# Kernel optimization log

Measured on AMD Instinct MI355X. Metric: run time of the kernel, lower is better.

## Reference

```python
import jax, jax.numpy as jnp
import numpy as np

SCALES = (5, 15, 40)


def _hamilton(a, b):
    # a, b: (..., 4) quaternions in [w, x, y, z]
    aw, ax, ay, az = a[..., 0], a[..., 1], a[..., 2], a[..., 3]
    bw, bx, by, bz = b[..., 0], b[..., 1], b[..., 2], b[..., 3]
    return jnp.stack([
        aw * bw - ax * bx - ay * by - az * bz,
        aw * bx + ax * bw + ay * bz - az * by,
        aw * by - ax * bz + ay * bw + az * bx,
        aw * bz + ax * by - ay * bx + az * bw,
    ], axis=-1)


def _bearing_quaternions(xyz):
    # xyz: (B, F, P, 3) -> bearing quaternions (B, F, P, 4)
    bbox_min = xyz.min(axis=2)
    bbox_max = xyz.max(axis=2)
    centroids = (bbox_min + bbox_max) * 0.5  # (B, F, 3)
    d = xyz - centroids[:, :, None, :]
    d = d / jnp.clip(jnp.linalg.norm(d, axis=-1, keepdims=True), 1e-12)
    dot = jnp.clip(d[..., 1], -1.0 + 1e-7, 1.0 - 1e-7)
    half = jnp.arccos(dot) * 0.5
    axis = jnp.stack([d[..., 2], jnp.zeros_like(d[..., 0]), -d[..., 0]], axis=-1)
    axis = axis / jnp.clip(jnp.linalg.norm(axis, axis=-1, keepdims=True), 1e-12)
    s = jnp.sin(half)
    return jnp.stack([jnp.cos(half), axis[..., 0] * s, axis[..., 1] * s, axis[..., 2] * s], axis=-1)


def _torch_lower_median(x):
    flat = jnp.sort(x.reshape(-1))
    return flat[(flat.shape[0] - 1) // 2]


def _bearing_qcc_multiscale(points_4d, num_frames):
    B, F, P, _ = points_4d.shape
    xyz = points_4d[..., :3]  # (B, F, P, 3)
    bq = _bearing_quaternions(xyz)  # (B, F, P, 4)

    # Per-transition relative quaternion q_fwd = q_tgt * conj(q_src), vectorized over T = F-1
    conj_sign = jnp.array([1.0, -1.0, -1.0, -1.0], dtype=points_4d.dtype)
    q_src = bq[:, :-1] * conj_sign  # conj, (B, T, P, 4)
    q_tgt = bq[:, 1:]
    q_fwd = _hamilton(q_tgt, q_src)
    q_fwd = q_fwd / jnp.clip(jnp.linalg.norm(q_fwd, axis=-1, keepdims=True), 1e-12)

    # KNN on source-frame xyz for all transitions at once (topk is sorted desc,
    # so smaller-k neighborhoods are prefixes of the max-k result)
    pts = xyz[:, :-1]  # (B, T, P, 3)
    sq = jnp.sum(pts * pts, axis=-1)  # (B, T, P)
    neg_dist = 2.0 * jnp.einsum('btpc,btqc->btpq', pts, pts) - sq[..., :, None] - sq[..., None, :]
    kmax = max(SCALES)
    _, idx = jax.lax.top_k(neg_dist, kmax)  # (B, T, P, kmax)

    # Gather neighbor quaternions: (B, T, P, kmax, 4)
    b_ix = jnp.arange(B)[:, None, None, None]
    t_ix = jnp.arange(F - 1)[None, :, None, None]
    nbr_q = q_fwd[b_ix, t_ix, idx]

    dots = jnp.abs(jnp.sum(q_fwd[..., None, :] * nbr_q, axis=-1))
    dots = jnp.clip(dots, 0.0, 1.0 - 1e-7)
    geo = 2.0 * jnp.arccos(dots)  # (B, T, P, kmax)

    rigidities = []
    for k in SCALES:
        mean_inc = geo[..., :k].mean(axis=-1).mean(axis=1)  # (B, P)
        scale = jnp.clip(_torch_lower_median(mean_inc), 1e-6)
        rig = jnp.where(mean_inc.max() > 0,
                        jnp.exp(-mean_inc / scale),
                        jnp.ones_like(mean_inc))  # (B, P)
        rig = jnp.broadcast_to(rig[:, None, :], (B, F, P)).reshape(B, 1, F * P)
        rigidities.append(rig)
    return jnp.concatenate(rigidities, axis=1)  # (B, len(SCALES), F*P)


def setup_inputs() -> dict:
    key = jax.random.key(0)
    B, F, P = 2, 8, 2048
    points_4d = jax.random.normal(key, (B, F, P, 4), dtype=jnp.float32)
    return {"points_4d": points_4d, "num_frames": F}


def reference(points_4d, num_frames):
    return _bearing_qcc_multiscale(points_4d, num_frames)
```

## Files before the change

kernel.cpp:

```cpp
#include <hip/hip_runtime.h>
#include <math.h>

typedef unsigned long long u64;
typedef unsigned int u32;

#define B_ 2
#define F_ 8
#define P_ 2048
#define T_ 7
#define ROWS (B_*T_*P_)
#define SENT_OU 0xFFFFFFFFu

#define CED(arr,a,b) do { double _x=arr[a], _y=arr[b]; arr[a]=fmin(_x,_y); arr[b]=fmax(_x,_y); } while(0)

__device__ __forceinline__ void sort8d(double* k) {
  CED(k,0,1); CED(k,2,3); CED(k,4,5); CED(k,6,7);
  CED(k,0,2); CED(k,1,3); CED(k,4,6); CED(k,5,7);
  CED(k,1,2); CED(k,5,6);
  CED(k,0,4); CED(k,1,5); CED(k,2,6); CED(k,3,7);
  CED(k,2,4); CED(k,3,5);
  CED(k,1,2); CED(k,3,4); CED(k,5,6);
}

__device__ __forceinline__ void low8(double* A, const double* Bv) {
#pragma unroll
  for (int i = 0; i < 8; ++i) A[i] = fmin(A[i], Bv[7-i]);
#pragma unroll
  for (int st = 4; st >= 1; st >>= 1) {
#pragma unroll
    for (int i = 0; i < 8; ++i) {
      if ((i & st) == 0) { CED(A, i, i + st); }
    }
  }
}

__device__ __forceinline__ u32 bfly16_min_u32(u32 x) {
  u32 t;
  t = (u32)__builtin_amdgcn_update_dpp((int)x,(int)x,0x0B1,0xF,0xF,false); x = t<x?t:x;
  t = (u32)__builtin_amdgcn_update_dpp((int)x,(int)x,0x04E,0xF,0xF,false); x = t<x?t:x;
  t = (u32)__builtin_amdgcn_update_dpp((int)x,(int)x,0x141,0xF,0xF,false); x = t<x?t:x;
  t = (u32)__builtin_amdgcn_update_dpp((int)x,(int)x,0x140,0xF,0xF,false); x = t<x?t:x;
  return x;
}
__device__ __forceinline__ float bfly16_sum_f32(float x) {
  float t;
  t = __uint_as_float((u32)__builtin_amdgcn_update_dpp((int)__float_as_uint(x),(int)__float_as_uint(x),0x0B1,0xF,0xF,false)); x += t;
  t = __uint_as_float((u32)__builtin_amdgcn_update_dpp((int)__float_as_uint(x),(int)__float_as_uint(x),0x04E,0xF,0xF,false)); x += t;
  t = __uint_as_float((u32)__builtin_amdgcn_update_dpp((int)__float_as_uint(x),(int)__float_as_uint(x),0x141,0xF,0xF,false)); x += t;
  t = __uint_as_float((u32)__builtin_amdgcn_update_dpp((int)__float_as_uint(x),(int)__float_as_uint(x),0x140,0xF,0xF,false)); x += t;
  return x;
}

__global__ __launch_bounds__(256) void kA1_bbox(const float4* __restrict__ pts,
                                                float* __restrict__ cent) {
  int bf = blockIdx.x;
  const float4* base = pts + (size_t)bf * P_;
  int tid = threadIdx.x;
  float mnx =  INFINITY, mny =  INFINITY, mnz =  INFINITY;
  float mxx = -INFINITY, mxy = -INFINITY, mxz = -INFINITY;
#pragma unroll
  for (int i = 0; i < 8; ++i) {
    float4 v = base[tid + i*256];
    mnx=fminf(mnx,v.x); mny=fminf(mny,v.y); mnz=fminf(mnz,v.z);
    mxx=fmaxf(mxx,v.x); mxy=fmaxf(mxy,v.y); mxz=fmaxf(mxz,v.z);
  }
#pragma unroll
  for (int off = 32; off >= 1; off >>= 1) {
    mnx=fminf(mnx,__shfl_xor(mnx,off)); mny=fminf(mny,__shfl_xor(mny,off)); mnz=fminf(mnz,__shfl_xor(mnz,off));
    mxx=fmaxf(mxx,__shfl_xor(mxx,off)); mxy=fmaxf(mxy,__shfl_xor(mxy,off)); mxz=fmaxf(mxz,__shfl_xor(mxz,off));
  }
  __shared__ float red[4][6];
  int wid = tid >> 6, lane = tid & 63;
  if (lane == 0) { red[wid][0]=mnx; red[wid][1]=mny; red[wid][2]=mnz;
                   red[wid][3]=mxx; red[wid][4]=mxy; red[wid][5]=mxz; }
  __syncthreads();
  if (tid == 0) {
    mnx=fminf(fminf(red[0][0],red[1][0]),fminf(red[2][0],red[3][0]));
    mny=fminf(fminf(red[0][1],red[1][1]),fminf(red[2][1],red[3][1]));
    mnz=fminf(fminf(red[0][2],red[1][2]),fminf(red[2][2],red[3][2]));
    mxx=fmaxf(fmaxf(red[0][3],red[1][3]),fmaxf(red[2][3],red[3][3]));
    mxy=fmaxf(fmaxf(red[0][4],red[1][4]),fmaxf(red[2][4],red[3][4]));
    mxz=fmaxf(fmaxf(red[0][5],red[1][5]),fmaxf(red[2][5],red[3][5]));
    cent[bf*3 + 0] = (mnx+mxx)*0.5f;
    cent[bf*3 + 1] = (mny+mxy)*0.5f;
    cent[bf*3 + 2] = (mnz+mxz)*0.5f;
  }
}

__device__ __forceinline__ float4 bearing(float4 v, float cx, float cy, float cz) {
  float dx=v.x-cx, dy=v.y-cy, dz=v.z-cz;
  float n = sqrtf(((dx*dx) + dy*dy) + dz*dz);
  n = fmaxf(n, 1e-12f);
  float dxn = dx/n, dyn = dy/n, dzn = dz/n;
  float dotc = fminf(fmaxf(dyn, -0.99999990f), 0.99999990f);
  float half = acosf(dotc) * 0.5f;
  float an = sqrtf(dzn*dzn + dxn*dxn);
  an = fmaxf(an, 1e-12f);
  float axx = dzn/an, axz = (-dxn)/an;
  float s = sinf(half), w = cosf(half);
  return make_float4(w, axx*s, 0.f, axz*s);
}

__global__ __launch_bounds__(256) void kAB_qfwd(const float4* __restrict__ pts,
                                                const float* __restrict__ cent,
                                                float4* __restrict__ qf,
                                                float4* __restrict__ pts2) {
  int i = blockIdx.x*256 + threadIdx.x;
  int p = i & (P_-1);
  int t = (i >> 11) % T_;
  int b = i / (T_*P_);
  int bf0 = b*F_ + t;
  float4 v0 = pts[(size_t)bf0*P_ + p];
  float4 v1 = pts[(size_t)(bf0+1)*P_ + p];
  float4 s = bearing(v0, cent[bf0*3+0], cent[bf0*3+1], cent[bf0*3+2]);
  float4 a = bearing(v1, cent[(bf0+1)*3+0], cent[(bf0+1)*3+1], cent[(bf0+1)*3+2]);
  float aw=a.x, ax=a.y, ay=a.z, az=a.w;
  float bw=s.x, bx=-s.y, by=-s.z, bz=-s.w;
  float w  = ((aw*bw - ax*bx) - ay*by) - az*bz;
  float xo = ((aw*bx + ax*bw) + ay*bz) - az*by;
  float yo = ((aw*by - ax*bz) + ay*bw) + az*bx;
  float zo = ((aw*bz + ax*by) - ay*bx) + az*bw;
  float n = sqrtf(((w*w + xo*xo) + yo*yo) + zo*zo);
  n = fmaxf(n, 1e-12f);
  qf[i] = make_float4(w/n, xo/n, yo/n, zo/n);
  float qs = fmaf(v0.x,v0.x, fmaf(v0.y,v0.y, v0.z*v0.z));
  pts2[(size_t)bf0*P_ + p] = make_float4(v0.x, v0.y, v0.z, qs);
}

__device__ __forceinline__ double mkkey(float4 c, u32 q,
                                        float px, float py, float pz, float ps) {
  float dot = fmaf(px, c.x, fmaf(py, c.y, pz*c.z));
  float nd  = fmaf(-2.f, dot, ps + c.w);
  return __hiloint2double(__float_as_int(nd), (int)q);
}
__device__ __forceinline__ u64 mkkey_u(float4 c, u32 q,
                                       float px, float py, float pz, float ps) {
  float dot = fmaf(px, c.x, fmaf(py, c.y, pz*c.z));
  float nd  = fmaf(-2.f, dot, ps + c.w);
  u32 u = __float_as_uint(nd);
  u32 ou = u ^ (((u32)((int)u >> 31)) | 0x80000000u);
  return ((u64)ou << 16) | q;
}

__device__ __forceinline__ void popstep(u32 (&OU)[8], u32 (&IX)[8],
                                        u32& LOU, u32& LIX, u32& CAP, int imod,
                                        int slot, const float4* __restrict__ pbase,
                                        float px, float py, float pz, float ps) {
  if (__any(OU[0] == SENT_OU)) {
    bool need = (OU[0] == SENT_OU);
    u64 lastK = ((u64)LOU << 16) | LIX;
    u64 best = ~0ull;
    for (int j = 0; j < 128; ++j) {
      u32 q = (u32)(j*16 + slot);
      u64 kk = mkkey_u(pbase[q], q, px,py,pz,ps);
      if (kk > lastK && kk < best) best = kk;
    }
    if (need && best != ~0ull) {
      OU[0] = (u32)(best >> 16); IX[0] = (u32)(best & 0xffffu);
      LOU = OU[0]; LIX = IX[0];
    }
  }
  u32 qmin = bfly16_min_u32(OU[0]);
  bool meq = (OU[0] == qmin);
  u32 tt   = meq ? IX[0] : 0xFFFFFFFFu;
  u32 widx = bfly16_min_u32(tt);
  bool iam = meq && (IX[0] == widx);
  CAP = (slot == imod) ? widx : CAP;
#pragma unroll
  for (int jj = 0; jj < 7; ++jj) {
    OU[jj] = iam ? OU[jj+1] : OU[jj];
    IX[jj] = iam ? IX[jj+1] : IX[jj];
  }
  OU[7] = iam ? SENT_OU : OU[7];
}

__global__ __launch_bounds__(256) void kC_select(const float4* __restrict__ pts2,
                                                 const float4* __restrict__ qf,
                                                 float* __restrict__ S) {
  int lane = threadIdx.x & 63;
  int wid  = threadIdx.x >> 6;
  int slot = lane & 15;
  int quarter = lane >> 4;
  int gid = blockIdx.x * 16 + wid * 4;
  int p0 = gid & (P_-1);
  int bt = gid >> 11;
  int t  = bt % T_;
  int b  = bt / T_;
  const float4* pbase = pts2 + (size_t)(b*F_ + t) * P_;

  int prow = p0 + quarter;
  float4 pw = pbase[prow];
  float px=pw.x, py=pw.y, pz=pw.z, ps=pw.w;

  double acc[8];
  {
    double k0[8];
#pragma unroll
    for (int u = 0; u < 8; ++u) { float4 c = pbase[u*16 + slot];
      k0[u] = mkkey(c, (u32)(u*16 + slot), px,py,pz,ps); }
    sort8d(k0);
#pragma unroll
    for (int j = 0; j < 8; ++j) acc[j] = k0[j];
  }
#pragma unroll 2
  for (int batch = 1; batch < 16; ++batch) {
    int qb = batch*128 + slot;
    float4 c[8];
#pragma unroll
    for (int u = 0; u < 8; ++u) c[u] = pbase[qb + u*16];
    double k[8];
#pragma unroll
    for (int u = 0; u < 8; ++u) k[u] = mkkey(c[u], (u32)(qb + u*16), px,py,pz,ps);
    sort8d(k);
    low8(acc, k);
  }

  u32 OU[8], IX[8];
#pragma unroll
  for (int j = 0; j < 8; ++j) {
    u64 bb = (u64)__double_as_longlong(acc[j]);
    u32 hi = (u32)(bb >> 32);
    OU[j] = hi ^ (((u32)((int)hi >> 31)) | 0x80000000u);
    IX[j] = (u32)(bb & 0xffffu);
  }
  u32 lou = OU[7], lix = IX[7];
  u32 cap1=0, cap2=0, cap3=0;

#pragma unroll 1
  for (int i = 0; i < 16; ++i)
    popstep(OU, IX, lou, lix, cap1, i, slot, pbase, px,py,pz,ps);
#pragma unroll 1
  for (int i = 0; i < 16; ++i)
    popstep(OU, IX, lou, lix, cap2, i, slot, pbase, px,py,pz,ps);
#pragma unroll 1
  for (int i = 0; i < 8; ++i)
    popstep(OU, IX, lou, lix, cap3, i, slot, pbase, px,py,pz,ps);

  int row = bt*P_ + prow;
  const float4* qbt = qf + (size_t)bt * P_;
  float4 qp = qf[row];

  float4 n; float d;
  n = qbt[cap1]; d = ((qp.x*n.x + qp.y*n.y) + qp.z*n.z) + qp.w*n.w;
  float g1 = 2.f * acosf(fminf(fabsf(d), 0.99999990f));
  n = qbt[cap2]; d = ((qp.x*n.x + qp.y*n.y) + qp.z*n.z) + qp.w*n.w;
  float g2 = 2.f * acosf(fminf(fabsf(d), 0.99999990f));
  n = qbt[cap3]; d = ((qp.x*n.x + qp.y*n.y) + qp.z*n.z) + qp.w*n.w;
  float g3 = (slot < 8) ? 2.f * acosf(fminf(fabsf(d), 0.99999990f)) : 0.f;

  float s40 = bfly16_sum_f32(g1 + g2 + g3);
  float s15 = bfly16_sum_f32((slot < 15) ? g1 : 0.f);
  float s5  = bfly16_sum_f32((slot < 5)  ? g1 : 0.f);

  if (slot == 0) {
    S[0*ROWS + row] = s5  / 5.f;
    S[1*ROWS + row] = s15 / 15.f;
    S[2*ROWS + row] = s40 / 40.f;
  }
}

__global__ __launch_bounds__(1024) void kE_final(const float* __restrict__ S,
                                                 float* __restrict__ out) {
  int k = blockIdx.x;
  int tid = threadIdx.x;
  __shared__ float srt[4096];
  const float* Sk = S + (size_t)k * ROWS;
  float m[4];
#pragma unroll
  for (int u = 0; u < 4; ++u) {
    int j = tid + u*1024;
    int b = j >> 11, p = j & 2047;
    float acc = 0.f;
#pragma unroll
    for (int t = 0; t < 7; ++t) acc += Sk[(b*7 + t)*2048 + p];
    m[u] = acc / 7.f;
    srt[j] = m[u];
  }
  __syncthreads();
  for (int size = 2; size <= 4096; size <<= 1) {
    for (int stride = size >> 1; stride > 0; stride >>= 1) {
      for (int c = tid; c < 2048; c += 1024) {
        int i = 2*c - (c & (stride - 1));
        int j = i + stride;
        bool up = ((i & size) == 0);
        float a = srt[i], bb = srt[j];
        if ((a > bb) == up) { srt[i] = bb; srt[j] = a; }
      }
      __syncthreads();
    }
  }
  float scale = fmaxf(srt[2047], 1e-6f);
  bool pos = srt[4095] > 0.f;
#pragma unroll
  for (int u = 0; u < 4; ++u) {
    int j = tid + u*1024;
    int b = j >> 11, p = j & 2047;
    float r = pos ? expf(-m[u]/scale) : 1.f;
    float* ob = out + ((size_t)(b*3 + k)*8)*2048 + p;
#pragma unroll
    for (int f = 0; f < 8; ++f) ob[f*2048] = r;
  }
}

extern "C" void kernel_launch(void* const* d_in, const int* in_sizes, int n_in,
                              void* d_out, int out_size, void* d_ws, size_t ws_size,
                              hipStream_t stream) {
  (void)in_sizes; (void)n_in; (void)out_size; (void)ws_size;
  const float4* pts = (const float4*)d_in[0];
  float* ws = (float*)d_ws;
  float4* qfw  = (float4*)ws;
  float*  S    = ws + 114688;
  float4* pts2 = (float4*)(ws + 114688 + 86016);
  float*  cent = ws + 114688 + 86016 + 131072;
  float*  out = (float*)d_out;

  hipLaunchKernelGGL(kA1_bbox,  dim3(B_*F_), dim3(256), 0, stream, pts, cent);
  hipLaunchKernelGGL(kAB_qfwd,  dim3(ROWS/256), dim3(256), 0, stream, pts, cent, (float4*)qfw, pts2);
  hipLaunchKernelGGL(kC_select, dim3(ROWS/16), dim3(256), 0, stream, pts2, qfw, S);
  hipLaunchKernelGGL(kE_final,  dim3(3), dim3(1024), 0, stream, S, out);
}
```

Baseline: 125.9 us.

## Replace bitonic sort median with radix-select and split mean computation kernel

The final stage used to sort 4096 means per scale with a shared-memory bitonic sort of about 78 barrier-separated passes just to read the median and the max. It now finds the lower median with a 4-pass 8-bit radix select over order-preserving integer keys, and gets the max from a wave-shuffle reduction. The per-point means over T are moved into a separate 48-block kernel so the 7-way gather runs across more CUs. This adds a kernel launch and a workspace buffer, and the serial per-pass histogram scan in thread 0 is a small cost.

Measured after the change: 155.2 us. +23.3%, slower.

```diff
diff --git a/kernel.cpp b/kernel.cpp
--- a/kernel.cpp
+++ b/kernel.cpp
@@ -259,46 +259,90 @@
   }
 }
 
-__global__ __launch_bounds__(1024) void kE_final(const float* __restrict__ S,
-                                                 float* __restrict__ out) {
+__global__ __launch_bounds__(256) void kE1_means(const float* __restrict__ S,
+                                                 float* __restrict__ M) {
+  int gid = blockIdx.x*256 + threadIdx.x;
+  int k = gid >> 12;
+  int j = gid & 4095;
+  int b = j >> 11, p = j & 2047;
+  const float* Sk = S + (size_t)k * ROWS;
+  float acc = 0.f;
+#pragma unroll
+  for (int t = 0; t < 7; ++t) acc += Sk[(b*7 + t)*2048 + p];
+  M[gid] = acc / 7.f;
+}
+
+__global__ __launch_bounds__(1024) void kE2_select(const float* __restrict__ M,
+                                                   float* __restrict__ out) {
   int k = blockIdx.x;
   int tid = threadIdx.x;
-  __shared__ float srt[4096];
-  const float* Sk = S + (size_t)k * ROWS;
-  float m[4];
+  __shared__ u32 hist[256];
+  __shared__ u32 sPref;
+  __shared__ int sRank;
+  __shared__ u32 sMax;
+  __shared__ u32 wmax[16];
+
+  float m[4]; u32 ou[4];
+#pragma unroll
+  for (int u = 0; u < 4; ++u) {
+    int j = tid + u*1024;
+    float v = M[k*4096 + j];
+    m[u] = v;
+    u32 bbits = __float_as_uint(v);
+    ou[u] = (bbits & 0x80000000u) ? ~bbits : (bbits | 0x80000000u);
+  }
+  u32 mx = ou[0] > ou[1] ? ou[0] : ou[1];
+  u32 mx2 = ou[2] > ou[3] ? ou[2] : ou[3];
+  mx = mx > mx2 ? mx : mx2;
+#pragma unroll
+  for (int off = 32; off >= 1; off >>= 1) {
+    u32 t = (u32)__shfl_xor((int)mx, off); mx = t > mx ? t : mx;
+  }
+  if ((tid & 63) == 0) wmax[tid >> 6] = mx;
+  if (tid == 0) { sPref = 0u; sRank = 2047; }
+  __syncthreads();
+  if (tid == 0) {
+    u32 g = wmax[0];
+#pragma unroll
+    for (int w = 1; w < 16; ++w) g = wmax[w] > g ? wmax[w] : g;
+    sMax = g;
+  }
+  for (int r = 0; r < 4; ++r) {
+    if (tid < 256) hist[tid] = 0u;
+    __syncthreads();
+    u32 pmask = (r == 0) ? 0u : (0xFFFFFFFFu << (32 - 8*r));
+    u32 pref = sPref;
+    int sh = 24 - 8*r;
+#pragma unroll
+    for (int u = 0; u < 4; ++u) {
+      if ((ou[u] & pmask) == pref)
+        atomicAdd(&hist[(ou[u] >> sh) & 255u], 1u);
+    }
+    __syncthreads();
+    if (tid == 0) {
+      int rk = sRank; u32 cum = 0;
+      for (int bb = 0; bb < 256; ++bb) {
+        u32 c = hist[bb];
+        if (cum + c > (u32)rk) { sPref = pref | ((u32)bb << sh); sRank = rk - (int)cum; break; }
+        cum += c;
+      }
+    }
+    __syncthreads();
+  }
+  u32 mou = sPref;
+  u32 mb  = (mou & 0x80000000u) ? (mou & 0x7FFFFFFFu) : ~mou;
+  float scale = fmaxf(__uint_as_float(mb), 1e-6f);
+  u32 xou = sMax;
+  u32 xb  = (xou & 0x80000000u) ? (xou & 0x7FFFFFFFu) : ~xou;
+  bool pos = __uint_as_float(xb) > 0.f;
 #pragma unroll
   for (int u = 0; u < 4; ++u) {
     int j = tid + u*1024;
     int b = j >> 11, p = j & 2047;
-    float acc = 0.f;
-#pragma unroll
-    for (int t = 0; t < 7; ++t) acc += Sk[(b*7 + t)*2048 + p];
-    m[u] = acc / 7.f;
-    srt[j] = m[u];
-  }
-  __syncthreads();
-  for (int size = 2; size <= 4096; size <<= 1) {
-    for (int stride = size >> 1; stride > 0; stride >>= 1) {
-      for (int c = tid; c < 2048; c += 1024) {
-        int i = 2*c - (c & (stride - 1));
-        int j = i + stride;
-        bool up = ((i & size) == 0);
-        float a = srt[i], bb = srt[j];
-        if ((a > bb) == up) { srt[i] = bb; srt[j] = a; }
-      }
-      __syncthreads();
-    }
-  }
-  float scale = fmaxf(srt[2047], 1e-6f);
-  bool pos = srt[4095] > 0.f;
-#pragma unroll
-  for (int u = 0; u < 4; ++u) {
-    int j = tid + u*1024;
-    int b = j >> 11, p = j & 2047;
-    float r = pos ? expf(-m[u]/scale) : 1.f;
+    float r_ = pos ? expf(-m[u]/scale) : 1.f;
     float* ob = out + ((size_t)(b*3 + k)*8)*2048 + p;
 #pragma unroll
-    for (int f = 0; f < 8; ++f) ob[f*2048] = r;
+    for (int f = 0; f < 8; ++f) ob[f*2048] = r_;
   }
 }
 
@@ -312,10 +356,12 @@
   float*  S    = ws + 114688;
   float4* pts2 = (float4*)(ws + 114688 + 86016);
   float*  cent = ws + 114688 + 86016 + 131072;
+  float*  M    = ws + 114688 + 86016 + 131072 + 48;
   float*  out = (float*)d_out;
 
-  hipLaunchKernelGGL(kA1_bbox,  dim3(B_*F_), dim3(256), 0, stream, pts, cent);
-  hipLaunchKernelGGL(kAB_qfwd,  dim3(ROWS/256), dim3(256), 0, stream, pts, cent, (float4*)qfw, pts2);
-  hipLaunchKernelGGL(kC_select, dim3(ROWS/16), dim3(256), 0, stream, pts2, qfw, S);
-  hipLaunchKernelGGL(kE_final,  dim3(3), dim3(1024), 0, stream, S, out);
-}
+  hipLaunchKernelGGL(kA1_bbox,   dim3(B_*F_), dim3(256), 0, stream, pts, cent);
+  hipLaunchKernelGGL(kAB_qfwd,   dim3(ROWS/256), dim3(256), 0, stream, pts, cent, (float4*)qfw, pts2);
+  hipLaunchKernelGGL(kC_select,  dim3(ROWS/16), dim3(256), 0, stream, pts2, qfw, S);
+  hipLaunchKernelGGL(kE1_means,  dim3(48), dim3(256), 0, stream, S, M);
+  hipLaunchKernelGGL(kE2_select, dim3(3), dim3(1024), 0, stream, M, out);
+}
```
